# Kernel tuning notes

Measured on AMD Instinct MI355X. Metric: run time of the kernel, lower is better.

Reference implementation:

```python
import jax, jax.numpy as jnp
import numpy as np

N_NODES = 50000
N_EDGES = 1600000
NFEAT, NHID, NCLASS = 512, 256, 64


def _mpnn_layer(x, src, dst, W, b, num_nodes):
    # linear transform then mean aggregation over incoming edges (incl. self loops)
    h = x @ W + b                      # [N, out]
    msg = h[src]                       # gather along edges [E+N, out]
    agg = jax.ops.segment_sum(msg, dst, num_segments=num_nodes)
    ones = jnp.ones((src.shape[0],), dtype=x.dtype)
    cnt = jax.ops.segment_sum(ones, dst, num_segments=num_nodes)
    return agg / jnp.maximum(cnt, 1.0)[:, None]


def setup_inputs() -> dict:
    key = jax.random.key(0)
    k1, k2, k3, k4, k5, k6 = jax.random.split(key, 6)
    x = jax.random.normal(k1, (N_NODES, NFEAT), dtype=jnp.float32)
    edge_index = jax.random.randint(k2, (2, N_EDGES), 0, N_NODES, dtype=jnp.int64)
    W1 = jax.random.normal(k3, (NFEAT, NHID), dtype=jnp.float32) * (1.0 / np.sqrt(NFEAT))
    b1 = jax.random.normal(k4, (NHID,), dtype=jnp.float32) * 0.01
    W2 = jax.random.normal(k5, (NHID, NCLASS), dtype=jnp.float32) * (1.0 / np.sqrt(NHID))
    b2 = jax.random.normal(k6, (NCLASS,), dtype=jnp.float32) * 0.01
    return {"x": x, "edge_index": edge_index, "W1": W1, "b1": b1, "W2": W2, "b2": b2}


def reference(x, edge_index, W1, b1, W2, b2):
    n = x.shape[0]
    # add self loops (done once per layer in the original; edge set identical)
    loops = jnp.arange(n, dtype=edge_index.dtype)
    src = jnp.concatenate([edge_index[0], loops])
    dst = jnp.concatenate([edge_index[1], loops])

    h = _mpnn_layer(x, src, dst, W1, b1, n)
    h = jax.nn.relu(h)
    # dropout is identity at inference
    h = _mpnn_layer(h, src, dst, W2, b2, n)
    return jax.nn.log_softmax(h, axis=1)
```

## Files before the change

kernel.cpp:

```cpp
#include <hip/hip_runtime.h>
#include <math.h>

#define NN 50000
#define NE 1600000
#define NF 512
#define NH 256
#define NC 64
#define CAP 96
#define NBKT 98
#define BCAP 18432
#define G1_BLOCKS 391
#define P1_BLOCKS 196

typedef short bf16x8 __attribute__((ext_vector_type(8)));
typedef float f32x4  __attribute__((ext_vector_type(4)));
typedef float f32x2  __attribute__((ext_vector_type(2)));

__device__ __forceinline__ float bf2f(unsigned short u) {
    return __uint_as_float(((unsigned)u) << 16);
}
__device__ __forceinline__ unsigned short f2bf(float f) {
    unsigned u = __float_as_uint(f);
    unsigned r = (u + 0x7FFF + ((u >> 16) & 1)) >> 16;
    return (unsigned short)r;
}

__device__ __forceinline__ unsigned char f2e4m3(float f) {
#if __has_builtin(__builtin_amdgcn_cvt_pk_fp8_f32)
    int v = __builtin_amdgcn_cvt_pk_fp8_f32(f, f, 0, false);
    return (unsigned char)(v & 0xff);
#else
    unsigned u = __float_as_uint(f);
    unsigned s = (u >> 31) << 7;
    float a = fabsf(f);
    if (a >= 448.f) return (unsigned char)(s | 0x7E);
    int e32 = (int)((u >> 23) & 0xff) - 127;
    if (e32 < -6) {
        int m = (int)rintf(a * 512.f);
        return (unsigned char)(s | m);
    }
    unsigned mant = u & 0x7fffff;
    unsigned keep = mant >> 20;
    unsigned rest = mant & 0xfffff;
    if (rest > 0x80000 || (rest == 0x80000 && (keep & 1))) keep++;
    int e8 = e32 + 7;
    if (keep == 8) { keep = 0; e8++; }
    if (e8 >= 16 || (e8 == 15 && keep == 7)) return (unsigned char)(s | 0x7E);
    return (unsigned char)(s | (e8 << 3) | keep);
#endif
}

__device__ __forceinline__ void dec4(unsigned int u, float& x0, float& x1, float& x2, float& x3) {
#if __has_builtin(__builtin_amdgcn_cvt_pk_f32_fp8)
    f32x2 lo = __builtin_amdgcn_cvt_pk_f32_fp8(u, false);
    f32x2 hi = __builtin_amdgcn_cvt_pk_f32_fp8(u, true);
    x0 = lo[0]; x1 = lo[1]; x2 = hi[0]; x3 = hi[1];
#else
    float r[4];
    #pragma unroll
    for (int i = 0; i < 4; ++i) {
        unsigned b = (u >> (8 * i)) & 0xff;
        unsigned s = (b >> 7) & 1, e = (b >> 3) & 15, m = b & 7;
        float v = e ? __uint_as_float(((e + 120u) << 23) | (m << 20))
                    : (float)m * 0.001953125f;
        r[i] = s ? -v : v;
    }
    x0 = r[0]; x1 = r[1]; x2 = r[2]; x3 = r[3];
#endif
}

__global__ __launch_bounds__(256)
void prep(const float* __restrict__ W1, const float* __restrict__ W2,
          unsigned short* __restrict__ w1t, unsigned short* __restrict__ w2t,
          const int* __restrict__ ei, int2* __restrict__ pairs, int* __restrict__ cursor,
          unsigned char* __restrict__ h1f, unsigned short* __restrict__ h2b) {
    __shared__ int bcnt[NBKT];
    __shared__ int bpos[NBKT];
    const int b = blockIdx.x;
    const int t = threadIdx.x;
    if (b < NF) {
        w1t[(size_t)t * NF + b] = f2bf(W1[(size_t)b * NH + t]);
        return;
    }
    if (b < NF + NH) {
        const int k = b - NF;
        if (t < NC) w2t[(size_t)t * NH + k] = f2bf(W2[(size_t)k * NC + t]);
        return;
    }
    if (b == NF + NH + P1_BLOCKS) {
        if (t < 64) reinterpret_cast<unsigned int*>(h1f)[(size_t)NN * 64 + t] = 0u;
        if (t < 32) reinterpret_cast<unsigned int*>(h2b)[(size_t)NN * 32 + t] = 0u;
        return;
    }
    const int fb = b - NF - NH;
    const int base = fb * 8192;
    for (int i = t; i < NBKT; i += 256) bcnt[i] = 0;
    __syncthreads();
    int ds[32], ss[32];
    #pragma unroll
    for (int k = 0; k < 32; ++k) {
        const int e = base + k * 256 + t;
        if (e < NE) {
            ds[k] = ei[NE + e];
            ss[k] = ei[e];
            atomicAdd(&bcnt[ds[k] >> 9], 1);
        } else ds[k] = -1;
    }
    __syncthreads();
    for (int i = t; i < NBKT; i += 256) bpos[i] = atomicAdd(&cursor[i], bcnt[i]);
    __syncthreads();
    #pragma unroll
    for (int k = 0; k < 32; ++k) {
        if (ds[k] >= 0) {
            const int bkt = ds[k] >> 9;
            const int p = atomicAdd(&bcnt[bkt], -1) - 1;
            const int g = bpos[bkt] + p;
            if (g < BCAP) {
                int2 v; v.x = ds[k]; v.y = ss[k];
                pairs[(size_t)bkt * BCAP + g] = v;
            }
        }
    }
}

__global__ __launch_bounds__(512)
void gemm1_fill(const float* __restrict__ A, const unsigned short* __restrict__ BT,
                const float* __restrict__ bias, unsigned char* __restrict__ C,
                const int2* __restrict__ pairs, const int* __restrict__ cursor,
                int* __restrict__ deg, int* __restrict__ csr) {
    __shared__ unsigned short As[128][40];
    __shared__ unsigned short Bs[256][40];
    __shared__ int ldeg[512];
    const int tid = threadIdx.x;

    if (blockIdx.x >= G1_BLOCKS) {
        const int fb = blockIdx.x - G1_BLOCKS;
        const int nb = fb * 512;
        ldeg[tid] = 0;
        __syncthreads();
        int cnt = cursor[fb];
        if (cnt > BCAP) cnt = BCAP;
        const int2* pb = pairs + (size_t)fb * BCAP;
        for (int i = tid; i < cnt; i += 512) {
            const int2 e = pb[i];
            const int p = atomicAdd(&ldeg[e.x & 511], 1);
            if (p < CAP) csr[(size_t)e.x * CAP + p] = e.y;
        }
        __syncthreads();
        const int node = nb + tid;
        if (node < NN) {
            const int d = ldeg[tid];
            deg[node] = d;
            const int dc = min(d, CAP);
            const int pd = min((dc + 15) & ~15, CAP);
            for (int p = dc; p < pd; ++p) csr[(size_t)node * CAP + p] = NN;
        }
        return;
    }

    const int w    = tid >> 6, lane = tid & 63;
    const int wr   = w >> 2,   wc   = w & 3;
    const int bm   = blockIdx.x * 128;
    const int rl   = lane & 15;
    const int ko   = (lane >> 4) * 8;

    f32x4 acc[4][4] = {};

    for (int k0 = 0; k0 < NF; k0 += 32) {
        {
            const int row = tid >> 2;
            const int kc  = (tid & 3) * 8;
            const int gr  = bm + row;
            float4 v0 = make_float4(0.f, 0.f, 0.f, 0.f), v1 = v0;
            if (gr < NN) {
                const float4* p = reinterpret_cast<const float4*>(A + (size_t)gr * NF + k0 + kc);
                v0 = p[0]; v1 = p[1];
            }
            bf16x8 pk;
            pk[0] = (short)f2bf(v0.x); pk[1] = (short)f2bf(v0.y);
            pk[2] = (short)f2bf(v0.z); pk[3] = (short)f2bf(v0.w);
            pk[4] = (short)f2bf(v1.x); pk[5] = (short)f2bf(v1.y);
            pk[6] = (short)f2bf(v1.z); pk[7] = (short)f2bf(v1.w);
            *reinterpret_cast<bf16x8*>(&As[row][kc]) = pk;
        }
        {
            const int row = tid >> 1;
            const int kc  = (tid & 1) * 16;
            const bf16x8* p = reinterpret_cast<const bf16x8*>(BT + (size_t)row * NF + k0 + kc);
            *reinterpret_cast<bf16x8*>(&Bs[row][kc])     = p[0];
            *reinterpret_cast<bf16x8*>(&Bs[row][kc + 8]) = p[1];
        }
        __syncthreads();

        bf16x8 af[4], bfr[4];
        #pragma unroll
        for (int m = 0; m < 4; ++m)
            af[m] = *reinterpret_cast<const bf16x8*>(&As[wr * 64 + m * 16 + rl][ko]);
        #pragma unroll
        for (int n = 0; n < 4; ++n)
            bfr[n] = *reinterpret_cast<const bf16x8*>(&Bs[wc * 64 + n * 16 + rl][ko]);
        #pragma unroll
        for (int m = 0; m < 4; ++m)
            #pragma unroll
            for (int n = 0; n < 4; ++n)
                acc[m][n] = __builtin_amdgcn_mfma_f32_16x16x32_bf16(af[m], bfr[n], acc[m][n], 0, 0, 0);
        __syncthreads();
    }

    float bv[4];
    #pragma unroll
    for (int n = 0; n < 4; ++n) bv[n] = bias[wc * 64 + n * 16 + rl];
    #pragma unroll
    for (int m = 0; m < 4; ++m) {
        #pragma unroll
        for (int j = 0; j < 4; ++j) {
            const int row = bm + wr * 64 + m * 16 + (lane >> 4) * 4 + j;
            if (row < NN) {
                #pragma unroll
                for (int n = 0; n < 4; ++n) {
                    const int col = wc * 64 + n * 16 + rl;
                    C[(size_t)row * NH + col] = f2e4m3(acc[m][n][j] + bv[n]);
                }
            }
        }
    }
}

__global__ __launch_bounds__(256)
void gemm2_mfma(const unsigned short* __restrict__ A, const unsigned short* __restrict__ BT,
                const float* __restrict__ bias, unsigned short* __restrict__ C) {
    __shared__ unsigned short As[128][40];
    __shared__ unsigned short Bs[64][40];
    const int tid = threadIdx.x;
    const int w = tid >> 6, lane = tid & 63;
    const int bm = blockIdx.x * 128;
    const int rl = lane & 15, ko = (lane >> 4) * 8;

    f32x4 acc[2][4] = {};

    for (int k0 = 0; k0 < NH; k0 += 32) {
        #pragma unroll
        for (int h = 0; h < 2; ++h) {
            const int c = tid + h * 256;
            const int row = c >> 2, kc = (c & 3) * 8;
            const int gr = bm + row;
            bf16x8 v = {};
            if (gr < NN) v = *reinterpret_cast<const bf16x8*>(A + (size_t)gr * NH + k0 + kc);
            *reinterpret_cast<bf16x8*>(&As[row][kc]) = v;
        }
        {
            const int row = tid >> 2, kc = (tid & 3) * 8;
            *reinterpret_cast<bf16x8*>(&Bs[row][kc]) =
                *reinterpret_cast<const bf16x8*>(BT + (size_t)row * NH + k0 + kc);
        }
        __syncthreads();

        bf16x8 af[2], bfr[4];
        #pragma unroll
        for (int m = 0; m < 2; ++m)
            af[m] = *reinterpret_cast<const bf16x8*>(&As[w * 32 + m * 16 + rl][ko]);
        #pragma unroll
        for (int n = 0; n < 4; ++n)
            bfr[n] = *reinterpret_cast<const bf16x8*>(&Bs[n * 16 + rl][ko]);
        #pragma unroll
        for (int m = 0; m < 2; ++m)
            #pragma unroll
            for (int n = 0; n < 4; ++n)
                acc[m][n] = __builtin_amdgcn_mfma_f32_16x16x32_bf16(af[m], bfr[n], acc[m][n], 0, 0, 0);
        __syncthreads();
    }

    float bv[4];
    #pragma unroll
    for (int n = 0; n < 4; ++n) bv[n] = bias[n * 16 + rl];
    #pragma unroll
    for (int m = 0; m < 2; ++m) {
        #pragma unroll
        for (int j = 0; j < 4; ++j) {
            const int row = bm + w * 32 + m * 16 + (lane >> 4) * 4 + j;
            if (row < NN) {
                #pragma unroll
                for (int n = 0; n < 4; ++n)
                    C[(size_t)row * NC + n * 16 + rl] = f2bf(acc[m][n][j] + bv[n]);
            }
        }
    }
}

__global__ __launch_bounds__(256)
void agg_relu(const unsigned char* __restrict__ hf, const int* __restrict__ deg,
              const int* __restrict__ csr, unsigned short* __restrict__ o) {
    const int node = blockIdx.x * 4 + (threadIdx.x >> 6);
    const int lane = threadIdx.x & 63;
    if (node >= NN) return;
    const int dcnt = min(deg[node], CAP);
    const int pad = (dcnt + 15) & ~15;
    const unsigned int* hfu = reinterpret_cast<const unsigned int*>(hf);
    const size_t loff = lane;

    float a0, a1, a2, a3;
    dec4(hfu[(size_t)node * 64 + loff], a0, a1, a2, a3);

    #define LDA(EE) hfu[(size_t)csr[EE] * 64 + loff]
    #define ACCA(U) { float b0,b1,b2,b3; dec4(U,b0,b1,b2,b3); a0+=b0; a1+=b1; a2+=b2; a3+=b3; }
    int e = node * CAP;
    const int eend = e + pad;
    if (pad > 0) {
        unsigned u0=LDA(e+0),u1=LDA(e+1),u2=LDA(e+2),u3=LDA(e+3),
                 u4=LDA(e+4),u5=LDA(e+5),u6=LDA(e+6),u7=LDA(e+7),
                 u8=LDA(e+8),u9=LDA(e+9),u10=LDA(e+10),u11=LDA(e+11),
                 u12=LDA(e+12),u13=LDA(e+13),u14=LDA(e+14),u15=LDA(e+15);
        e += 16;
        for (; e < eend; e += 16) {
            unsigned t;
            t=LDA(e+0);  ACCA(u0)  u0=t;
            t=LDA(e+1);  ACCA(u1)  u1=t;
            t=LDA(e+2);  ACCA(u2)  u2=t;
            t=LDA(e+3);  ACCA(u3)  u3=t;
            t=LDA(e+4);  ACCA(u4)  u4=t;
            t=LDA(e+5);  ACCA(u5)  u5=t;
            t=LDA(e+6);  ACCA(u6)  u6=t;
            t=LDA(e+7);  ACCA(u7)  u7=t;
            t=LDA(e+8);  ACCA(u8)  u8=t;
            t=LDA(e+9);  ACCA(u9)  u9=t;
            t=LDA(e+10); ACCA(u10) u10=t;
            t=LDA(e+11); ACCA(u11) u11=t;
            t=LDA(e+12); ACCA(u12) u12=t;
            t=LDA(e+13); ACCA(u13) u13=t;
            t=LDA(e+14); ACCA(u14) u14=t;
            t=LDA(e+15); ACCA(u15) u15=t;
        }
        ACCA(u0) ACCA(u1) ACCA(u2) ACCA(u3) ACCA(u4) ACCA(u5) ACCA(u6) ACCA(u7)
        ACCA(u8) ACCA(u9) ACCA(u10) ACCA(u11) ACCA(u12) ACCA(u13) ACCA(u14) ACCA(u15)
    }
    #undef LDA
    #undef ACCA

    const float inv = 1.0f / (float)(dcnt + 1);
    ushort4 r;
    r.x = f2bf(fmaxf(a0 * inv, 0.f));
    r.y = f2bf(fmaxf(a1 * inv, 0.f));
    r.z = f2bf(fmaxf(a2 * inv, 0.f));
    r.w = f2bf(fmaxf(a3 * inv, 0.f));
    *reinterpret_cast<ushort4*>(o + (size_t)node * NH + lane * 4) = r;
}

__global__ __launch_bounds__(256)
void agg2_softmax(const unsigned short* __restrict__ h2, const int* __restrict__ deg,
                  const int* __restrict__ csr, float* __restrict__ out) {
    const int node = blockIdx.x * 8 + (threadIdx.x >> 5);
    const int l = threadIdx.x & 31;
    if (node >= NN) return;
    const int dcnt = min(deg[node], CAP);
    const int pad = (dcnt + 15) & ~15;
    const unsigned int* h2u = reinterpret_cast<const unsigned int*>(h2);

    unsigned int su = h2u[(size_t)node * 32 + l];
    float a0 = bf2f((unsigned short)(su & 0xffff));
    float a1 = bf2f((unsigned short)(su >> 16));

    #define LDB(EE) h2u[(size_t)csr[EE] * 32 + l]
    #define ACCB(U) { a0 += bf2f((unsigned short)((U) & 0xffff)); a1 += bf2f((unsigned short)((U) >> 16)); }
    int e = node * CAP;
    const int eend = e + pad;
    if (pad > 0) {
        unsigned u0=LDB(e+0),u1=LDB(e+1),u2=LDB(e+2),u3=LDB(e+3),
                 u4=LDB(e+4),u5=LDB(e+5),u6=LDB(e+6),u7=LDB(e+7),
                 u8=LDB(e+8),u9=LDB(e+9),u10=LDB(e+10),u11=LDB(e+11),
                 u12=LDB(e+12),u13=LDB(e+13),u14=LDB(e+14),u15=LDB(e+15);
        e += 16;
        for (; e < eend; e += 16) {
            unsigned t;
            t=LDB(e+0);  ACCB(u0)  u0=t;
            t=LDB(e+1);  ACCB(u1)  u1=t;
            t=LDB(e+2);  ACCB(u2)  u2=t;
            t=LDB(e+3);  ACCB(u3)  u3=t;
            t=LDB(e+4);  ACCB(u4)  u4=t;
            t=LDB(e+5);  ACCB(u5)  u5=t;
            t=LDB(e+6);  ACCB(u6)  u6=t;
            t=LDB(e+7);  ACCB(u7)  u7=t;
            t=LDB(e+8);  ACCB(u8)  u8=t;
            t=LDB(e+9);  ACCB(u9)  u9=t;
            t=LDB(e+10); ACCB(u10) u10=t;
            t=LDB(e+11); ACCB(u11) u11=t;
            t=LDB(e+12); ACCB(u12) u12=t;
            t=LDB(e+13); ACCB(u13) u13=t;
            t=LDB(e+14); ACCB(u14) u14=t;
            t=LDB(e+15); ACCB(u15) u15=t;
        }
        ACCB(u0) ACCB(u1) ACCB(u2) ACCB(u3) ACCB(u4) ACCB(u5) ACCB(u6) ACCB(u7)
        ACCB(u8) ACCB(u9) ACCB(u10) ACCB(u11) ACCB(u12) ACCB(u13) ACCB(u14) ACCB(u15)
    }
    #undef LDB
    #undef ACCB

    const float inv = 1.0f / (float)(dcnt + 1);
    a0 *= inv; a1 *= inv;

    float m = fmaxf(a0, a1);
    #pragma unroll
    for (int o = 16; o > 0; o >>= 1) m = fmaxf(m, __shfl_xor(m, o));
    float s = expf(a0 - m) + expf(a1 - m);
    #pragma unroll
    for (int o = 16; o > 0; o >>= 1) s += __shfl_xor(s, o);
    const float lg = logf(s);
    float2 r;
    r.x = a0 - m - lg;
    r.y = a1 - m - lg;
    *reinterpret_cast<float2*>(out + (size_t)node * NC + l * 2) = r;
}

extern "C" void kernel_launch(void* const* d_in, const int* in_sizes, int n_in,
                              void* d_out, int out_size, void* d_ws, size_t ws_size,
                              hipStream_t stream) {
    const float* x  = (const float*)d_in[0];
    const int*   ei = (const int*)d_in[1];
    const float* W1 = (const float*)d_in[2];
    const float* b1 = (const float*)d_in[3];
    const float* W2 = (const float*)d_in[4];
    const float* b2 = (const float*)d_in[5];
    float* out = (float*)d_out;

    char* ws = (char*)d_ws;
    unsigned short* hr     = (unsigned short*)(ws);
    unsigned char*  h1f    = (unsigned char*)(ws + 25600000);
    unsigned short* h2b    = (unsigned short*)(ws + 38400256);
    unsigned short* w1t    = (unsigned short*)(ws + 44800512);
    unsigned short* w2t    = (unsigned short*)(ws + 45062656);
    int*            deg    = (int*)(ws + 45095424);
    int*            csr    = (int*)(ws + 45295424);
    int2*           pairs  = (int2*)(ws + 64495424);
    int*            cursor = (int*)(ws + 78946112);

    hipMemsetAsync(cursor, 0, NBKT * sizeof(int), stream);

    prep<<<NF + NH + P1_BLOCKS + 1, 256, 0, stream>>>(W1, W2, w1t, w2t, ei, pairs, cursor, h1f, h2b);

    gemm1_fill<<<G1_BLOCKS + NBKT, 512, 0, stream>>>(x, w1t, b1, h1f, pairs, cursor, deg, csr);

    agg_relu<<<(NN + 3) / 4, 256, 0, stream>>>(h1f, deg, csr, hr);

    gemm2_mfma<<<(NN + 127) / 128, 256, 0, stream>>>(hr, w2t, b2, h2b);

    agg2_softmax<<<(NN + 7) / 8, 256, 0, stream>>>(h2b, deg, csr, out);
}
```

Baseline: 150.7 us.

## Halve prep edge chunk, deepen GEMM1 K-tile, pack two nodes per wave in agg

Three separate changes. The edge-bucketing prep pass now uses twice as many blocks with half the edges each. GEMM1 stages a 64-wide K slice per iteration instead of 32, halving barrier count at the cost of more shared memory. agg_relu now handles two nodes per 64-lane wave, each half-wave loading 8 fp8 bytes per lane with 8-deep prefetch. Because both halves loop to the larger padded degree, lanes of the shorter node load padding rows.

```diff
diff --git a/kernel.cpp b/kernel.cpp
--- a/kernel.cpp
+++ b/kernel.cpp
@@ -10,7 +10,7 @@
 #define NBKT 98
 #define BCAP 18432
 #define G1_BLOCKS 391
-#define P1_BLOCKS 196
+#define P1_BLOCKS 392
 
 typedef short bf16x8 __attribute__((ext_vector_type(8)));
 typedef float f32x4  __attribute__((ext_vector_type(4)));
@@ -93,12 +93,12 @@
         return;
     }
     const int fb = b - NF - NH;
-    const int base = fb * 8192;
+    const int base = fb * 4096;
     for (int i = t; i < NBKT; i += 256) bcnt[i] = 0;
     __syncthreads();
-    int ds[32], ss[32];
-    #pragma unroll
-    for (int k = 0; k < 32; ++k) {
+    int ds[16], ss[16];
+    #pragma unroll
+    for (int k = 0; k < 16; ++k) {
         const int e = base + k * 256 + t;
         if (e < NE) {
             ds[k] = ei[NE + e];
@@ -110,7 +110,7 @@
     for (int i = t; i < NBKT; i += 256) bpos[i] = atomicAdd(&cursor[i], bcnt[i]);
     __syncthreads();
     #pragma unroll
-    for (int k = 0; k < 32; ++k) {
+    for (int k = 0; k < 16; ++k) {
         if (ds[k] >= 0) {
             const int bkt = ds[k] >> 9;
             const int p = atomicAdd(&bcnt[bkt], -1) - 1;
@@ -128,8 +128,8 @@
                 const float* __restrict__ bias, unsigned char* __restrict__ C,
                 const int2* __restrict__ pairs, const int* __restrict__ cursor,
                 int* __restrict__ deg, int* __restrict__ csr) {
-    __shared__ unsigned short As[128][40];
-    __shared__ unsigned short Bs[256][40];
+    __shared__ unsigned short As[128][72];
+    __shared__ unsigned short Bs[256][72];
     __shared__ int ldeg[512];
     const int tid = threadIdx.x;
 
@@ -166,44 +166,54 @@
 
     f32x4 acc[4][4] = {};
 
-    for (int k0 = 0; k0 < NF; k0 += 32) {
+    for (int k0 = 0; k0 < NF; k0 += 64) {
         {
             const int row = tid >> 2;
-            const int kc  = (tid & 3) * 8;
+            const int kc  = (tid & 3) * 16;
             const int gr  = bm + row;
-            float4 v0 = make_float4(0.f, 0.f, 0.f, 0.f), v1 = v0;
+            float4 v0 = make_float4(0.f, 0.f, 0.f, 0.f), v1 = v0, v2 = v0, v3 = v0;
             if (gr < NN) {
                 const float4* p = reinterpret_cast<const float4*>(A + (size_t)gr * NF + k0 + kc);
-                v0 = p[0]; v1 = p[1];
+                v0 = p[0]; v1 = p[1]; v2 = p[2]; v3 = p[3];
             }
-            bf16x8 pk;
-            pk[0] = (short)f2bf(v0.x); pk[1] = (short)f2bf(v0.y);
-            pk[2] = (short)f2bf(v0.z); pk[3] = (short)f2bf(v0.w);
-            pk[4] = (short)f2bf(v1.x); pk[5] = (short)f2bf(v1.y);
-            pk[6] = (short)f2bf(v1.z); pk[7] = (short)f2bf(v1.w);
-            *reinterpret_cast<bf16x8*>(&As[row][kc]) = pk;
+            bf16x8 pk0, pk1;
+            pk0[0] = (short)f2bf(v0.x); pk0[1] = (short)f2bf(v0.y);
+            pk0[2] = (short)f2bf(v0.z); pk0[3] = (short)f2bf(v0.w);
+            pk0[4] = (short)f2bf(v1.x); pk0[5] = (short)f2bf(v1.y);
+            pk0[6] = (short)f2bf(v1.z); pk0[7] = (short)f2bf(v1.w);
+            pk1[0] = (short)f2bf(v2.x); pk1[1] = (short)f2bf(v2.y);
+            pk1[2] = (short)f2bf(v2.z); pk1[3] = (short)f2bf(v2.w);
+            pk1[4] = (short)f2bf(v3.x); pk1[5] = (short)f2bf(v3.y);
+            pk1[6] = (short)f2bf(v3.z); pk1[7] = (short)f2bf(v3.w);
+            *reinterpret_cast<bf16x8*>(&As[row][kc])     = pk0;
+            *reinterpret_cast<bf16x8*>(&As[row][kc + 8]) = pk1;
         }
         {
             const int row = tid >> 1;
-            const int kc  = (tid & 1) * 16;
+            const int kc  = (tid & 1) * 32;
             const bf16x8* p = reinterpret_cast<const bf16x8*>(BT + (size_t)row * NF + k0 + kc);
-            *reinterpret_cast<bf16x8*>(&Bs[row][kc])     = p[0];
-            *reinterpret_cast<bf16x8*>(&Bs[row][kc + 8]) = p[1];
-        }
-        __syncthreads();
-
-        bf16x8 af[4], bfr[4];
-        #pragma unroll
-        for (int m = 0; m < 4; ++m)
-            af[m] = *reinterpret_cast<const bf16x8*>(&As[wr * 64 + m * 16 + rl][ko]);
-        #pragma unroll
-        for (int n = 0; n < 4; ++n)
-            bfr[n] = *reinterpret_cast<const bf16x8*>(&Bs[wc * 64 + n * 16 + rl][ko]);
-        #pragma unroll
-        for (int m = 0; m < 4; ++m)
+            *reinterpret_cast<bf16x8*>(&Bs[row][kc])      = p[0];
+            *reinterpret_cast<bf16x8*>(&Bs[row][kc + 8])  = p[1];
+            *reinterpret_cast<bf16x8*>(&Bs[row][kc + 16]) = p[2];
+            *reinterpret_cast<bf16x8*>(&Bs[row][kc + 24]) = p[3];
+        }
+        __syncthreads();
+
+        #pragma unroll
+        for (int ks = 0; ks < 64; ks += 32) {
+            bf16x8 af[4], bfr[4];
+            #pragma unroll
+            for (int m = 0; m < 4; ++m)
+                af[m] = *reinterpret_cast<const bf16x8*>(&As[wr * 64 + m * 16 + rl][ks + ko]);
             #pragma unroll
             for (int n = 0; n < 4; ++n)
-                acc[m][n] = __builtin_amdgcn_mfma_f32_16x16x32_bf16(af[m], bfr[n], acc[m][n], 0, 0, 0);
+                bfr[n] = *reinterpret_cast<const bf16x8*>(&Bs[wc * 64 + n * 16 + rl][ks + ko]);
+            #pragma unroll
+            for (int m = 0; m < 4; ++m)
+                #pragma unroll
+                for (int n = 0; n < 4; ++n)
+                    acc[m][n] = __builtin_amdgcn_mfma_f32_16x16x32_bf16(af[m], bfr[n], acc[m][n], 0, 0, 0);
+        }
         __syncthreads();
     }
 
@@ -290,59 +300,60 @@
 __global__ __launch_bounds__(256)
 void agg_relu(const unsigned char* __restrict__ hf, const int* __restrict__ deg,
               const int* __restrict__ csr, unsigned short* __restrict__ o) {
-    const int node = blockIdx.x * 4 + (threadIdx.x >> 6);
-    const int lane = threadIdx.x & 63;
-    if (node >= NN) return;
-    const int dcnt = min(deg[node], CAP);
-    const int pad = (dcnt + 15) & ~15;
-    const unsigned int* hfu = reinterpret_cast<const unsigned int*>(hf);
-    const size_t loff = lane;
-
-    float a0, a1, a2, a3;
-    dec4(hfu[(size_t)node * 64 + loff], a0, a1, a2, a3);
-
-    #define LDA(EE) hfu[(size_t)csr[EE] * 64 + loff]
-    #define ACCA(U) { float b0,b1,b2,b3; dec4(U,b0,b1,b2,b3); a0+=b0; a1+=b1; a2+=b2; a3+=b3; }
-    int e = node * CAP;
-    const int eend = e + pad;
-    if (pad > 0) {
-        unsigned u0=LDA(e+0),u1=LDA(e+1),u2=LDA(e+2),u3=LDA(e+3),
-                 u4=LDA(e+4),u5=LDA(e+5),u6=LDA(e+6),u7=LDA(e+7),
-                 u8=LDA(e+8),u9=LDA(e+9),u10=LDA(e+10),u11=LDA(e+11),
-                 u12=LDA(e+12),u13=LDA(e+13),u14=LDA(e+14),u15=LDA(e+15);
-        e += 16;
-        for (; e < eend; e += 16) {
-            unsigned t;
-            t=LDA(e+0);  ACCA(u0)  u0=t;
-            t=LDA(e+1);  ACCA(u1)  u1=t;
-            t=LDA(e+2);  ACCA(u2)  u2=t;
-            t=LDA(e+3);  ACCA(u3)  u3=t;
-            t=LDA(e+4);  ACCA(u4)  u4=t;
-            t=LDA(e+5);  ACCA(u5)  u5=t;
-            t=LDA(e+6);  ACCA(u6)  u6=t;
-            t=LDA(e+7);  ACCA(u7)  u7=t;
-            t=LDA(e+8);  ACCA(u8)  u8=t;
-            t=LDA(e+9);  ACCA(u9)  u9=t;
-            t=LDA(e+10); ACCA(u10) u10=t;
-            t=LDA(e+11); ACCA(u11) u11=t;
-            t=LDA(e+12); ACCA(u12) u12=t;
-            t=LDA(e+13); ACCA(u13) u13=t;
-            t=LDA(e+14); ACCA(u14) u14=t;
-            t=LDA(e+15); ACCA(u15) u15=t;
-        }
-        ACCA(u0) ACCA(u1) ACCA(u2) ACCA(u3) ACCA(u4) ACCA(u5) ACCA(u6) ACCA(u7)
-        ACCA(u8) ACCA(u9) ACCA(u10) ACCA(u11) ACCA(u12) ACCA(u13) ACCA(u14) ACCA(u15)
-    }
-    #undef LDA
-    #undef ACCA
-
-    const float inv = 1.0f / (float)(dcnt + 1);
-    ushort4 r;
-    r.x = f2bf(fmaxf(a0 * inv, 0.f));
-    r.y = f2bf(fmaxf(a1 * inv, 0.f));
-    r.z = f2bf(fmaxf(a2 * inv, 0.f));
-    r.w = f2bf(fmaxf(a3 * inv, 0.f));
-    *reinterpret_cast<ushort4*>(o + (size_t)node * NH + lane * 4) = r;
+    const int tid = threadIdx.x;
+    const int w = tid >> 6, lane = tid & 63;
+    const int half = lane >> 5, l = lane & 31;
+    const int node = blockIdx.x * 8 + w * 2 + half;
+    const bool valid = node < NN;
+    const int nd = valid ? node : NN;
+    const int dcnt = valid ? min(deg[node], CAP) : 0;
+    const int pad  = (dcnt + 15) & ~15;
+    const int opad = __shfl_xor(pad, 32);
+    const int mx   = max(pad, opad);
+    const int beg  = min(nd, NN - 1) * CAP;
+    const uint2* hf2 = reinterpret_cast<const uint2*>(hf);
+
+    float a0, a1, a2, a3, a4, a5, a6, a7;
+    {
+        const uint2 s = hf2[(size_t)nd * 32 + l];
+        dec4(s.x, a0, a1, a2, a3);
+        dec4(s.y, a4, a5, a6, a7);
+    }
+
+    #define IDX1(J) (((J) < pad) ? csr[beg + (J)] : NN)
+    #define LD1(J)  hf2[(size_t)IDX1(J) * 32 + l]
+    #define ACC1(U) { float b0,b1,b2,b3; dec4((U).x,b0,b1,b2,b3); a0+=b0; a1+=b1; a2+=b2; a3+=b3; \
+                      dec4((U).y,b0,b1,b2,b3); a4+=b0; a5+=b1; a6+=b2; a7+=b3; }
+
+    if (mx > 0) {
+        uint2 u0=LD1(0),u1=LD1(1),u2=LD1(2),u3=LD1(3),
+              u4=LD1(4),u5=LD1(5),u6=LD1(6),u7=LD1(7);
+        for (int e = 8; e < mx; e += 8) {
+            uint2 t;
+            t=LD1(e+0); ACC1(u0) u0=t;
+            t=LD1(e+1); ACC1(u1) u1=t;
+            t=LD1(e+2); ACC1(u2) u2=t;
+            t=LD1(e+3); ACC1(u3) u3=t;
+            t=LD1(e+4); ACC1(u4) u4=t;
+            t=LD1(e+5); ACC1(u5) u5=t;
+            t=LD1(e+6); ACC1(u6) u6=t;
+            t=LD1(e+7); ACC1(u7) u7=t;
+        }
+        ACC1(u0) ACC1(u1) ACC1(u2) ACC1(u3) ACC1(u4) ACC1(u5) ACC1(u6) ACC1(u7)
+    }
+    #undef IDX1
+    #undef LD1
+    #undef ACC1
+
+    if (valid) {
+        const float inv = 1.0f / (float)(dcnt + 1);
+        uint4 r;
+        r.x = (unsigned)f2bf(fmaxf(a0 * inv, 0.f)) | ((unsigned)f2bf(fmaxf(a1 * inv, 0.f)) << 16);
+        r.y = (unsigned)f2bf(fmaxf(a2 * inv, 0.f)) | ((unsigned)f2bf(fmaxf(a3 * inv, 0.f)) << 16);
+        r.z = (unsigned)f2bf(fmaxf(a4 * inv, 0.f)) | ((unsigned)f2bf(fmaxf(a5 * inv, 0.f)) << 16);
+        r.w = (unsigned)f2bf(fmaxf(a6 * inv, 0.f)) | ((unsigned)f2bf(fmaxf(a7 * inv, 0.f)) << 16);
+        *reinterpret_cast<uint4*>(o + (size_t)node * NH + l * 8) = r;
+    }
 }
 
 __global__ __launch_bounds__(256)
@@ -438,7 +449,7 @@
 
     gemm1_fill<<<G1_BLOCKS + NBKT, 512, 0, stream>>>(x, w1t, b1, h1f, pairs, cursor, deg, csr);
 
-    agg_relu<<<(NN + 3) / 4, 256, 0, stream>>>(h1f, deg, csr, hr);
+    agg_relu<<<(NN + 7) / 8, 256, 0, stream>>>(h1f, deg, csr, hr);
 
     gemm2_mfma<<<(NN + 127) / 128, 256, 0, stream>>>(hr, w2t, b2, h2b);
 
```

Result: slower. 182.1 us (+20.9%).
